# Performance work log

Measured on AMD Instinct MI355X. Metric: run time of the kernel, lower is better.

Reference implementation:

```python
import jax, jax.numpy as jnp
import numpy as np

B, S, HID = 8, 2048, 1024
H, DH = 16, 64
EPS = 1e-12  # torch F.normalize eps


def _heads(x):
    # [B,S,HID] -> [B,H,S,DH]
    return x.reshape(B, S, H, DH).transpose(0, 2, 1, 3)


def _l2norm(x):
    n = jnp.sqrt(jnp.sum(x * x, axis=-1, keepdims=True))
    return x / jnp.maximum(n, EPS)


def setup_inputs() -> dict:
    key = jax.random.key(0)
    ks = jax.random.split(key, 4)
    sc = 0.02
    return {
        "hidden_states": jax.random.normal(ks[0], (B, S, HID), jnp.float32),
        "attention_mask": jnp.zeros((B, 1, 1, S), jnp.int32),
        "Wq": jax.random.normal(ks[1], (HID, HID), jnp.float32) * sc,
        "bq": jnp.zeros((HID,), jnp.float32),
        "Wk": jax.random.normal(ks[2], (HID, HID), jnp.float32) * sc,
        "bk": jnp.zeros((HID,), jnp.float32),
        "Wv": jax.random.normal(ks[3], (HID, HID), jnp.float32) * sc,
        "bv": jnp.zeros((HID,), jnp.float32),
    }


def reference(hidden_states, attention_mask, Wq, bq, Wk, bk, Wv, bv):
    # QKV projections (nn.Linear: x @ W^T + b; here W stored as [in,out]-equivalent square)
    q = _heads(hidden_states @ Wq + bq)  # [B,H,S,DH]
    k = _heads(hidden_states @ Wk + bk)
    v = _heads(hidden_states @ Wv + bv)

    # mask == 0 -> valid token; transpose(-1,-2): [B,1,1,S] -> [B,1,S,1]
    mask = (attention_mask == 0).astype(q.dtype)            # [B,1,1,S]
    mask_t = jnp.swapaxes(mask, -1, -2)                      # [B,1,S,1]
    q = q * mask_t
    k = k * mask_t
    v = v * mask_t

    q = _l2norm(q)
    k = _l2norm(k)
    v = v / mask.sum(-1)[..., None]                          # divide by valid-token count

    if q.shape[-1] > q.shape[-2]:
        # DH > S: explicit O(S^2) path
        ctx = jnp.einsum("bhsq,bhqd->bhsd", jnp.einsum("bhse,bhqe->bhsq", q, k), v)
    else:
        # linear-attention order: Q @ (K^T V), O(S*DH^2)
        kv = jnp.einsum("bhse,bhsd->bhed", k, v)             # [B,H,DH,DH]
        ctx = jnp.einsum("bhse,bhed->bhsd", q, kv)

    return ctx.transpose(0, 2, 1, 3).reshape(B, S, HID)
```

## Files before the change

kernel.cpp:

```cpp
#include <hip/hip_runtime.h>
#include <stdint.h>

#define B_    8
#define S_    2048
#define HID_  1024
#define H_    16
#define DH_   64
#define M_    (B_ * S_)

using bf16x8 = __attribute__((ext_vector_type(8))) __bf16;
using bf16x4 = __attribute__((ext_vector_type(4))) __bf16;
using f32x4  = __attribute__((ext_vector_type(4))) float;

__device__ __forceinline__ void gload_lds16(const void* g, void* l) {
  __builtin_amdgcn_global_load_lds(
      (const __attribute__((address_space(1))) void*)g,
      (__attribute__((address_space(3))) void*)l, 16, 0, 0);
}

__global__ void cast_hs(const float* __restrict__ hs, __bf16* __restrict__ out, int n8) {
  int i = blockIdx.x * blockDim.x + threadIdx.x;
  int stride = gridDim.x * blockDim.x;
  for (; i < n8; i += stride) {
    const float4* p = (const float4*)(hs + (size_t)i * 8);
    float4 a = p[0], c = p[1];
    bf16x8 v;
    v[0] = (__bf16)a.x; v[1] = (__bf16)a.y; v[2] = (__bf16)a.z; v[3] = (__bf16)a.w;
    v[4] = (__bf16)c.x; v[5] = (__bf16)c.y; v[6] = (__bf16)c.z; v[7] = (__bf16)c.w;
    *(bf16x8*)(out + (size_t)i * 8) = v;
  }
}

__global__ void transpose_w(const float* __restrict__ Wq, const float* __restrict__ Wk,
                            const float* __restrict__ Wv, __bf16* __restrict__ Wt) {
  __shared__ float tile[32][33];
  int w = blockIdx.z;
  const float* W = (w == 0) ? Wq : (w == 1) ? Wk : Wv;
  int k0 = blockIdx.x * 32, n0 = blockIdx.y * 32;
  int tx = threadIdx.x, ty = threadIdx.y;
#pragma unroll
  for (int i = 0; i < 4; ++i)
    tile[ty * 4 + i][tx] = W[(size_t)(k0 + ty * 4 + i) * HID_ + n0 + tx];
  __syncthreads();
#pragma unroll
  for (int i = 0; i < 4; ++i)
    Wt[(size_t)w * HID_ * HID_ + (size_t)(n0 + ty * 4 + i) * HID_ + k0 + tx] =
        (__bf16)tile[tx][ty * 4 + i];
}

__global__ void mask_prep(const int* __restrict__ mask, float* __restrict__ validf,
                          float* __restrict__ counts) {
  __shared__ float red[256];
  int b = blockIdx.x;
  float cnt = 0.f;
  for (int s = threadIdx.x; s < S_; s += 256) {
    float v = (mask[b * S_ + s] == 0) ? 1.f : 0.f;
    validf[b * S_ + s] = v;
    cnt += v;
  }
  red[threadIdx.x] = cnt;
  __syncthreads();
  for (int off = 128; off > 0; off >>= 1) {
    if (threadIdx.x < off) red[threadIdx.x] += red[threadIdx.x + off];
    __syncthreads();
  }
  if (threadIdx.x == 0) counts[b] = red[0];
}

__global__ __launch_bounds__(512, 2) void qkv_gemm8(
    const __bf16* __restrict__ hsb, const __bf16* __restrict__ Wt,
    const float* __restrict__ biasq, const float* __restrict__ biask,
    const float* __restrict__ biasv, const float* __restrict__ validf,
    const float* __restrict__ counts, __bf16* __restrict__ qn,
    __bf16* __restrict__ kT, __bf16* __restrict__ vT) {
  __shared__ __bf16 As[2][2][128 * 64];
  __shared__ __bf16 Bs[2][2][128 * 64];

  int bid = blockIdx.x;
  int swz = (bid & 7) * 96 + (bid >> 3);
  int tm = swz / 12;
  int tnw = swz - tm * 12;
  int tn = tnw & 3;
  int w  = tnw >> 2;

  int tid = threadIdx.x;
  int lane = tid & 63, wid = tid >> 6;
  int lr = lane & 15, g = lane >> 4;
  int wr = wid >> 2, wcn = wid & 3;

  int m0 = tm * 256, n0 = tn * 256;
  const __bf16* Bsrc = Wt + (size_t)w * (HID_ * HID_);

  int srow = tid >> 3;
  int scol = ((tid & 7) ^ (srow & 7)) << 3;
  int soff = tid * 16;

  auto stA = [&](int t_, int ah) {
    const __bf16* s0 = hsb + (size_t)(m0 + ah * 128 + srow) * HID_ + t_ * 64 + scol;
    char* d = (char*)&As[t_ & 1][ah][0] + soff;
    gload_lds16(s0, d);
    gload_lds16(s0 + (size_t)64 * HID_, d + 8192);
  };
  auto stB = [&](int t_, int bh) {
    const __bf16* s0 = Bsrc + (size_t)(n0 + bh * 128 + srow) * HID_ + t_ * 64 + scol;
    char* d = (char*)&Bs[t_ & 1][bh][0] + soff;
    gload_lds16(s0, d);
    gload_lds16(s0 + (size_t)64 * HID_, d + 8192);
  };

  int swz8 = (lr & 7) << 4;
  int arow = wr * 64 + lr;
  int brow = (wcn & 1) * 64 + lr;
  int bsel = wcn >> 1;

  f32x4 acc[8][4] = {};
  bf16x8 fb[4], fbN[4], fa0[4], fa1[4];

#define RD_A(DST, BUF, MH, KK)                                                \
  _Pragma("unroll")                                                           \
  for (int mf = 0; mf < 4; ++mf)                                              \
    DST[mf] = *(const bf16x8*)((const char*)&As[BUF][MH][0] +                 \
                               (arow + mf * 16) * 128 +                       \
                               (((KK) * 64 + g * 16) ^ swz8));                \
  __builtin_amdgcn_sched_barrier(0);

#define RD_B(DST, BUF, KK)                                                    \
  _Pragma("unroll")                                                           \
  for (int nf = 0; nf < 4; ++nf)                                              \
    DST[nf] = *(const bf16x8*)((const char*)&Bs[BUF][bsel][0] +               \
                               (brow + nf * 16) * 128 +                       \
                               (((KK) * 64 + g * 16) ^ swz8));                \
  __builtin_amdgcn_sched_barrier(0);

#define CLUSTER(ACCB, FA, FB, LG)                                             \
  asm volatile("s_waitcnt lgkmcnt(" #LG ")" ::: "memory");                    \
  __builtin_amdgcn_sched_barrier(0);                                          \
  __builtin_amdgcn_s_setprio(1);                                              \
  _Pragma("unroll")                                                           \
  for (int mf = 0; mf < 4; ++mf)                                              \
    _Pragma("unroll")                                                         \
    for (int nf = 0; nf < 4; ++nf)                                            \
      acc[(ACCB) + mf][nf] = __builtin_amdgcn_mfma_f32_16x16x32_bf16(         \
          FA[mf], FB[nf], acc[(ACCB) + mf][nf], 0, 0, 0);                     \
  __builtin_amdgcn_s_setprio(0);                                              \
  __builtin_amdgcn_sched_barrier(0);

  stA(0, 0); stA(0, 1); stB(0, 0); stB(0, 1);

#pragma unroll 2
  for (int t = 0; t < 16; ++t) {
    int buf = t & 1;
    asm volatile("s_waitcnt vmcnt(0)" ::: "memory");
    __builtin_amdgcn_s_barrier();
    __builtin_amdgcn_sched_barrier(0);

    RD_B(fb,  buf, 0);
    RD_A(fa0, buf, 0, 0);
    RD_A(fa1, buf, 1, 0);
    if (t < 15) { stA(t + 1, 0); stA(t + 1, 1); }

    CLUSTER(0, fa0, fb, 4)

    RD_B(fbN, buf, 1);
    RD_A(fa0, buf, 0, 1);
    if (t < 15) stB(t + 1, 0);

    CLUSTER(4, fa1, fb, 8)

    RD_A(fa1, buf, 1, 1);
    if (t < 15) stB(t + 1, 1);

    CLUSTER(0, fa0, fbN, 4)
    CLUSTER(4, fa1, fbN, 0)
  }
#undef RD_A
#undef RD_B
#undef CLUSTER

  const float* bias = (w == 0) ? biasq : (w == 1) ? biask : biasv;
  float bb[4];
#pragma unroll
  for (int nf = 0; nf < 4; ++nf) bb[nf] = bias[n0 + wcn * 64 + nf * 16 + lr];

  int batch = m0 >> 11;
  float invcnt = 1.0f / counts[batch];
  int h = tn * 4 + wcn;

#pragma unroll
  for (int m = 0; m < 8; ++m) {
    int mh = m >> 2, mf = m & 3;
    int rbase = m0 + mh * 128 + wr * 64 + mf * 16 + g * 4;
    float vld[4];
#pragma unroll
    for (int j = 0; j < 4; ++j) vld[j] = validf[rbase + j];
    float ss[4] = {0.f, 0.f, 0.f, 0.f};
#pragma unroll
    for (int nf = 0; nf < 4; ++nf)
#pragma unroll
      for (int j = 0; j < 4; ++j) {
        float x = (acc[m][nf][j] + bb[nf]) * vld[j];
        acc[m][nf][j] = x;
        ss[j] += x * x;
      }
    float sc[4];
#pragma unroll
    for (int j = 0; j < 4; ++j) {
      float s = ss[j];
      s += __shfl_xor(s, 1);
      s += __shfl_xor(s, 2);
      s += __shfl_xor(s, 4);
      s += __shfl_xor(s, 8);
      if (w == 2) sc[j] = vld[j] * invcnt;
      else        sc[j] = 1.0f / fmaxf(sqrtf(s), 1e-12f);
    }
    if (w == 0) {
#pragma unroll
      for (int nf = 0; nf < 4; ++nf) {
        int c = n0 + wcn * 64 + nf * 16 + lr;
#pragma unroll
        for (int j = 0; j < 4; ++j)
          qn[(size_t)(rbase + j) * HID_ + c] = (__bf16)(acc[m][nf][j] * sc[j]);
      }
    } else {
      __bf16* dst = (w == 1) ? kT : vT;
      int sbase = rbase & (S_ - 1);
#pragma unroll
      for (int nf = 0; nf < 4; ++nf) {
        int d = nf * 16 + lr;
        bf16x4 pk;
#pragma unroll
        for (int j = 0; j < 4; ++j) pk[j] = (__bf16)(acc[m][nf][j] * sc[j]);
        *(bf16x4*)(dst + (size_t)((batch * H_ + h) * DH_ + d) * S_ + sbase) = pk;
      }
    }
  }
}

__global__ __launch_bounds__(256) void kv_gemm(const __bf16* __restrict__ kT,
                                               const __bf16* __restrict__ vT,
                                               __bf16* __restrict__ vk) {
  __shared__ __align__(16) char smem[65536];
  __bf16* kbuf = (__bf16*)smem;
  __bf16* vbuf = (__bf16*)(smem + 32768);

  int bh = blockIdx.x;
  int tid = threadIdx.x, lane = tid & 63, wid = tid >> 6;
  int g = lane >> 4, lr = lane & 15;
  const __bf16* kb = kT + (size_t)bh * DH_ * S_;
  const __bf16* vb = vT + (size_t)bh * DH_ * S_;

  f32x4 acc[4][4] = {};

  for (int sc0 = 0; sc0 < S_; sc0 += 256) {
#pragma unroll
    for (int it = 0; it < 8; ++it) {
      int seg = tid + it * 256;
      int row = seg >> 5, col = (seg & 31) * 8;
      gload_lds16(kb + (size_t)row * S_ + sc0 + col, (void*)(kbuf + seg * 8));
      gload_lds16(vb + (size_t)row * S_ + sc0 + col, (void*)(vbuf + seg * 8));
    }
    __syncthreads();
    int sl = wid * 64;
#pragma unroll
    for (int kk = 0; kk < 64; kk += 32) {
      bf16x8 fa[4], fb[4];
#pragma unroll
      for (int m = 0; m < 4; ++m)
        fa[m] = *(const bf16x8*)(vbuf + (m * 16 + lr) * 256 + sl + kk + g * 8);
#pragma unroll
      for (int n = 0; n < 4; ++n)
        fb[n] = *(const bf16x8*)(kbuf + (n * 16 + lr) * 256 + sl + kk + g * 8);
#pragma unroll
      for (int m = 0; m < 4; ++m)
#pragma unroll
        for (int n = 0; n < 4; ++n)
          acc[m][n] = __builtin_amdgcn_mfma_f32_16x16x32_bf16(fa[m], fb[n], acc[m][n], 0, 0, 0);
    }
    __syncthreads();
  }

  float* red = (float*)smem;
#pragma unroll
  for (int m = 0; m < 4; ++m)
#pragma unroll
    for (int n = 0; n < 4; ++n)
#pragma unroll
      for (int j = 0; j < 4; ++j)
        red[wid * 4096 + (m * 16 + g * 4 + j) * 64 + n * 16 + lr] = acc[m][n][j];
  __syncthreads();
  for (int idx = tid; idx < 4096; idx += 256) {
    float s = red[idx] + red[4096 + idx] + red[8192 + idx] + red[12288 + idx];
    vk[(size_t)bh * 4096 + idx] = (__bf16)s;
  }
}

__global__ __launch_bounds__(256) void ctx_gemm(const __bf16* __restrict__ qn,
                                                const __bf16* __restrict__ vk,
                                                float* __restrict__ out) {
  __shared__ __align__(16) __bf16 qbuf[128 * 64];
  __shared__ __align__(16) __bf16 wbuf[64 * 64];

  int st = blockIdx.x;
  int bh = blockIdx.y;
  int b = bh >> 4, h = bh & 15;
  int tid = threadIdx.x, lane = tid & 63, wid = tid >> 6;
  int g = lane >> 4, lr = lane & 15;
  int s0 = st * 128;

#pragma unroll
  for (int it = 0; it < 4; ++it) {
    int seg = tid + it * 256;
    int row = seg >> 3, col = (seg & 7) * 8;
    gload_lds16(qn + (size_t)(b * S_ + s0 + row) * HID_ + h * DH_ + col,
                (void*)(qbuf + seg * 8));
  }
#pragma unroll
  for (int it = 0; it < 2; ++it) {
    int seg = tid + it * 256;
    gload_lds16(vk + (size_t)bh * 4096 + seg * 8, (void*)(wbuf + seg * 8));
  }
  __syncthreads();

  f32x4 acc[2][4] = {};
#pragma unroll
  for (int kk = 0; kk < 64; kk += 32) {
    bf16x8 fa[2], fb[4];
#pragma unroll
    for (int m = 0; m < 2; ++m)
      fa[m] = *(const bf16x8*)(qbuf + (wid * 32 + m * 16 + lr) * 64 + kk + g * 8);
#pragma unroll
    for (int n = 0; n < 4; ++n)
      fb[n] = *(const bf16x8*)(wbuf + (n * 16 + lr) * 64 + kk + g * 8);
#pragma unroll
    for (int m = 0; m < 2; ++m)
#pragma unroll
      for (int n = 0; n < 4; ++n)
        acc[m][n] = __builtin_amdgcn_mfma_f32_16x16x32_bf16(fa[m], fb[n], acc[m][n], 0, 0, 0);
  }

#pragma unroll
  for (int m = 0; m < 2; ++m) {
    int rbase = s0 + wid * 32 + m * 16 + g * 4;
#pragma unroll
    for (int n = 0; n < 4; ++n) {
      int d = n * 16 + lr;
#pragma unroll
      for (int j = 0; j < 4; ++j)
        out[(size_t)(b * S_ + rbase + j) * HID_ + h * DH_ + d] = acc[m][n][j];
    }
  }
}

extern "C" void kernel_launch(void* const* d_in, const int* in_sizes, int n_in,
                              void* d_out, int out_size, void* d_ws, size_t ws_size,
                              hipStream_t stream) {
  const float* hs   = (const float*)d_in[0];
  const int*   mask = (const int*)d_in[1];
  const float* Wq   = (const float*)d_in[2];
  const float* bq   = (const float*)d_in[3];
  const float* Wk   = (const float*)d_in[4];
  const float* bk   = (const float*)d_in[5];
  const float* Wv   = (const float*)d_in[6];
  const float* bv   = (const float*)d_in[7];
  float* out = (float*)d_out;

  char* ws = (char*)d_ws;
  __bf16* hsb    = (__bf16*)(ws);
  __bf16* Wt     = (__bf16*)(ws + (33554432));
  __bf16* qn     = (__bf16*)(ws + (41943040));
  __bf16* kT     = (__bf16*)(ws + (75497472));
  __bf16* vT     = (__bf16*)(ws + (109051904));
  __bf16* vk     = (__bf16*)(ws + (142606336));
  float*  validf = (float*)(ws + (143654912));
  float*  counts = (float*)(ws + (143654912) + 65536);

  cast_hs<<<2048, 256, 0, stream>>>(hs, hsb, (B_ * S_ * HID_) / 8);
  transpose_w<<<dim3(32, 32, 3), dim3(32, 8), 0, stream>>>(Wq, Wk, Wv, Wt);
  mask_prep<<<8, 256, 0, stream>>>(mask, validf, counts);
  qkv_gemm8<<<768, 512, 0, stream>>>(hsb, Wt, bq, bk, bv, validf, counts, qn, kT, vT);
  kv_gemm<<<128, 256, 0, stream>>>(kT, vT, vk);
  ctx_gemm<<<dim3(16, 128), 256, 0, stream>>>(qn, vk, out);
}
```

Before: 184.9 us.

## Load GEMM B operand directly to registers and split kv_gemm over sequence halves

```diff
diff --git a/kernel.cpp b/kernel.cpp
--- a/kernel.cpp
+++ b/kernel.cpp
@@ -74,7 +74,6 @@
     const float* __restrict__ counts, __bf16* __restrict__ qn,
     __bf16* __restrict__ kT, __bf16* __restrict__ vT) {
   __shared__ __bf16 As[2][2][128 * 64];
-  __shared__ __bf16 Bs[2][2][128 * 64];
 
   int bid = blockIdx.x;
   int swz = (bid & 7) * 96 + (bid >> 3);
@@ -101,20 +100,17 @@
     gload_lds16(s0, d);
     gload_lds16(s0 + (size_t)64 * HID_, d + 8192);
   };
-  auto stB = [&](int t_, int bh) {
-    const __bf16* s0 = Bsrc + (size_t)(n0 + bh * 128 + srow) * HID_ + t_ * 64 + scol;
-    char* d = (char*)&Bs[t_ & 1][bh][0] + soff;
-    gload_lds16(s0, d);
-    gload_lds16(s0 + (size_t)64 * HID_, d + 8192);
-  };
 
   int swz8 = (lr & 7) << 4;
   int arow = wr * 64 + lr;
-  int brow = (wcn & 1) * 64 + lr;
-  int bsel = wcn >> 1;
+
+  const __bf16* bp[4];
+#pragma unroll
+  for (int nf = 0; nf < 4; ++nf)
+    bp[nf] = Bsrc + (size_t)(n0 + wcn * 64 + nf * 16 + lr) * HID_ + g * 8;
 
   f32x4 acc[8][4] = {};
-  bf16x8 fb[4], fbN[4], fa0[4], fa1[4];
+  bf16x8 fa[4], fab[4], fbX[4], fbY[4], fbN[4];
 
 #define RD_A(DST, BUF, MH, KK)                                                \
   _Pragma("unroll")                                                           \
@@ -124,15 +120,7 @@
                                (((KK) * 64 + g * 16) ^ swz8));                \
   __builtin_amdgcn_sched_barrier(0);
 
-#define RD_B(DST, BUF, KK)                                                    \
-  _Pragma("unroll")                                                           \
-  for (int nf = 0; nf < 4; ++nf)                                              \
-    DST[nf] = *(const bf16x8*)((const char*)&Bs[BUF][bsel][0] +               \
-                               (brow + nf * 16) * 128 +                       \
-                               (((KK) * 64 + g * 16) ^ swz8));                \
-  __builtin_amdgcn_sched_barrier(0);
-
-#define CLUSTER(ACCB, FA, FB, LG)                                             \
+#define CLUSTER(ACCB, FA, FB, LG)                                            \
   asm volatile("s_waitcnt lgkmcnt(" #LG ")" ::: "memory");                    \
   __builtin_amdgcn_sched_barrier(0);                                          \
   __builtin_amdgcn_s_setprio(1);                                              \
@@ -145,37 +133,44 @@
   __builtin_amdgcn_s_setprio(0);                                              \
   __builtin_amdgcn_sched_barrier(0);
 
-  stA(0, 0); stA(0, 1); stB(0, 0); stB(0, 1);
-
-#pragma unroll 2
-  for (int t = 0; t < 16; ++t) {
-    int buf = t & 1;
-    asm volatile("s_waitcnt vmcnt(0)" ::: "memory");
-    __builtin_amdgcn_s_barrier();
-    __builtin_amdgcn_sched_barrier(0);
-
-    RD_B(fb,  buf, 0);
-    RD_A(fa0, buf, 0, 0);
-    RD_A(fa1, buf, 1, 0);
-    if (t < 15) { stA(t + 1, 0); stA(t + 1, 1); }
-
-    CLUSTER(0, fa0, fb, 4)
-
-    RD_B(fbN, buf, 1);
-    RD_A(fa0, buf, 0, 1);
-    if (t < 15) stB(t + 1, 0);
-
-    CLUSTER(4, fa1, fb, 8)
-
-    RD_A(fa1, buf, 1, 1);
-    if (t < 15) stB(t + 1, 1);
-
-    CLUSTER(0, fa0, fbN, 4)
-    CLUSTER(4, fa1, fbN, 0)
+#define STEP(T, BUF, FBC, FBP)                                                \
+  {                                                                           \
+    asm volatile("s_waitcnt vmcnt(0)" ::: "memory");                          \
+    __builtin_amdgcn_s_barrier();                                             \
+    __builtin_amdgcn_sched_barrier(0);                                        \
+    _Pragma("unroll")                                                         \
+    for (int nf = 0; nf < 4; ++nf)                                            \
+      fbN[nf] = *(const bf16x8*)(bp[nf] + (T) * 64 + 32);                     \
+    __builtin_amdgcn_sched_barrier(0);                                        \
+    RD_A(fa,  BUF, 0, 0)                                                      \
+    RD_A(fab, BUF, 0, 1)                                                      \
+    if ((T) < 15) stA((T) + 1, 0);                                            \
+    CLUSTER(0, fa, FBC, 4)                                                    \
+    CLUSTER(0, fab, fbN, 0)                                                   \
+    RD_A(fa,  BUF, 1, 0)                                                      \
+    RD_A(fab, BUF, 1, 1)                                                      \
+    if ((T) < 15) {                                                           \
+      stA((T) + 1, 1);                                                        \
+      _Pragma("unroll")                                                       \
+      for (int nf = 0; nf < 4; ++nf)                                          \
+        FBP[nf] = *(const bf16x8*)(bp[nf] + ((T) + 1) * 64);                  \
+    }                                                                         \
+    __builtin_amdgcn_sched_barrier(0);                                        \
+    CLUSTER(4, fa, FBC, 4)                                                    \
+    CLUSTER(4, fab, fbN, 0)                                                   \
+  }
+
+  stA(0, 0); stA(0, 1);
+#pragma unroll
+  for (int nf = 0; nf < 4; ++nf) fbX[nf] = *(const bf16x8*)(bp[nf]);
+
+  for (int t2 = 0; t2 < 16; t2 += 2) {
+    STEP(t2,     0, fbX, fbY)
+    STEP(t2 + 1, 1, fbY, fbX)
   }
 #undef RD_A
-#undef RD_B
 #undef CLUSTER
+#undef STEP
 
   const float* bias = (w == 0) ? biasq : (w == 1) ? biask : biasv;
   float bb[4];
@@ -238,12 +233,12 @@
 
 __global__ __launch_bounds__(256) void kv_gemm(const __bf16* __restrict__ kT,
                                                const __bf16* __restrict__ vT,
-                                               __bf16* __restrict__ vk) {
+                                               float* __restrict__ vkp) {
   __shared__ __align__(16) char smem[65536];
   __bf16* kbuf = (__bf16*)smem;
   __bf16* vbuf = (__bf16*)(smem + 32768);
 
-  int bh = blockIdx.x;
+  int bh = blockIdx.x & 127, half = blockIdx.x >> 7;
   int tid = threadIdx.x, lane = tid & 63, wid = tid >> 6;
   int g = lane >> 4, lr = lane & 15;
   const __bf16* kb = kT + (size_t)bh * DH_ * S_;
@@ -251,7 +246,8 @@
 
   f32x4 acc[4][4] = {};
 
-  for (int sc0 = 0; sc0 < S_; sc0 += 256) {
+  int sbeg = half * (S_ / 2);
+  for (int sc0 = sbeg; sc0 < sbeg + S_ / 2; sc0 += 256) {
 #pragma unroll
     for (int it = 0; it < 8; ++it) {
       int seg = tid + it * 256;
@@ -290,8 +286,14 @@
   __syncthreads();
   for (int idx = tid; idx < 4096; idx += 256) {
     float s = red[idx] + red[4096 + idx] + red[8192 + idx] + red[12288 + idx];
-    vk[(size_t)bh * 4096 + idx] = (__bf16)s;
-  }
+    vkp[(size_t)(half * 128 + bh) * 4096 + idx] = s;
+  }
+}
+
+__global__ __launch_bounds__(256) void vk_reduce(const float* __restrict__ vkp,
+                                                 __bf16* __restrict__ vk) {
+  int i = blockIdx.x * 256 + threadIdx.x;
+  vk[i] = (__bf16)(vkp[i] + vkp[524288 + i]);
 }
 
 __global__ __launch_bounds__(256) void ctx_gemm(const __bf16* __restrict__ qn,
@@ -373,11 +375,13 @@
   __bf16* vk     = (__bf16*)(ws + (142606336));
   float*  validf = (float*)(ws + (143654912));
   float*  counts = (float*)(ws + (143654912) + 65536);
+  float*  vkp    = (float*)(ws + (33554432));
 
   cast_hs<<<2048, 256, 0, stream>>>(hs, hsb, (B_ * S_ * HID_) / 8);
   transpose_w<<<dim3(32, 32, 3), dim3(32, 8), 0, stream>>>(Wq, Wk, Wv, Wt);
   mask_prep<<<8, 256, 0, stream>>>(mask, validf, counts);
   qkv_gemm8<<<768, 512, 0, stream>>>(hsb, Wt, bq, bk, bv, validf, counts, qn, kT, vT);
-  kv_gemm<<<128, 256, 0, stream>>>(kT, vT, vk);
+  kv_gemm<<<256, 256, 0, stream>>>(kT, vT, vkp);
+  vk_reduce<<<2048, 256, 0, stream>>>(vkp, vk);
   ctx_gemm<<<dim3(16, 128), 256, 0, stream>>>(qn, vk, out);
 }
```

New measurement: 223.8 us, median of 4. 21.0% more time.

## Merge prep kernels into one launch and split kv_gemm over sequence halves

Applied to the files above, without the earlier changes.

```diff
diff --git a/kernel.cpp b/kernel.cpp
--- a/kernel.cpp
+++ b/kernel.cpp
@@ -18,53 +18,58 @@
       (__attribute__((address_space(3))) void*)l, 16, 0, 0);
 }
 
-__global__ void cast_hs(const float* __restrict__ hs, __bf16* __restrict__ out, int n8) {
-  int i = blockIdx.x * blockDim.x + threadIdx.x;
-  int stride = gridDim.x * blockDim.x;
-  for (; i < n8; i += stride) {
-    const float4* p = (const float4*)(hs + (size_t)i * 8);
-    float4 a = p[0], c = p[1];
-    bf16x8 v;
-    v[0] = (__bf16)a.x; v[1] = (__bf16)a.y; v[2] = (__bf16)a.z; v[3] = (__bf16)a.w;
-    v[4] = (__bf16)c.x; v[5] = (__bf16)c.y; v[6] = (__bf16)c.z; v[7] = (__bf16)c.w;
-    *(bf16x8*)(out + (size_t)i * 8) = v;
-  }
-}
-
-__global__ void transpose_w(const float* __restrict__ Wq, const float* __restrict__ Wk,
-                            const float* __restrict__ Wv, __bf16* __restrict__ Wt) {
-  __shared__ float tile[32][33];
-  int w = blockIdx.z;
-  const float* W = (w == 0) ? Wq : (w == 1) ? Wk : Wv;
-  int k0 = blockIdx.x * 32, n0 = blockIdx.y * 32;
-  int tx = threadIdx.x, ty = threadIdx.y;
-#pragma unroll
-  for (int i = 0; i < 4; ++i)
-    tile[ty * 4 + i][tx] = W[(size_t)(k0 + ty * 4 + i) * HID_ + n0 + tx];
-  __syncthreads();
-#pragma unroll
-  for (int i = 0; i < 4; ++i)
-    Wt[(size_t)w * HID_ * HID_ + (size_t)(n0 + ty * 4 + i) * HID_ + k0 + tx] =
-        (__bf16)tile[tx][ty * 4 + i];
-}
-
-__global__ void mask_prep(const int* __restrict__ mask, float* __restrict__ validf,
-                          float* __restrict__ counts) {
-  __shared__ float red[256];
-  int b = blockIdx.x;
-  float cnt = 0.f;
-  for (int s = threadIdx.x; s < S_; s += 256) {
-    float v = (mask[b * S_ + s] == 0) ? 1.f : 0.f;
-    validf[b * S_ + s] = v;
-    cnt += v;
-  }
-  red[threadIdx.x] = cnt;
-  __syncthreads();
-  for (int off = 128; off > 0; off >>= 1) {
-    if (threadIdx.x < off) red[threadIdx.x] += red[threadIdx.x + off];
+__global__ __launch_bounds__(256) void prep(
+    const float* __restrict__ hs, __bf16* __restrict__ hsb,
+    const float* __restrict__ Wq, const float* __restrict__ Wk,
+    const float* __restrict__ Wv, __bf16* __restrict__ Wt,
+    const int* __restrict__ mask, float* __restrict__ validf,
+    float* __restrict__ counts) {
+  int bid = blockIdx.x;
+  int tid = threadIdx.x;
+  if (bid < 2048) {
+    int n8 = (B_ * S_ * HID_) / 8;
+    int i = bid * 256 + tid;
+    int stride = 2048 * 256;
+    for (; i < n8; i += stride) {
+      const float4* p = (const float4*)(hs + (size_t)i * 8);
+      float4 a = p[0], c = p[1];
+      bf16x8 v;
+      v[0] = (__bf16)a.x; v[1] = (__bf16)a.y; v[2] = (__bf16)a.z; v[3] = (__bf16)a.w;
+      v[4] = (__bf16)c.x; v[5] = (__bf16)c.y; v[6] = (__bf16)c.z; v[7] = (__bf16)c.w;
+      *(bf16x8*)(hsb + (size_t)i * 8) = v;
+    }
+  } else if (bid < 5120) {
+    __shared__ float tile[32][33];
+    int idx = bid - 2048;
+    int w = idx >> 10, r = idx & 1023;
+    int k0 = (r & 31) * 32, n0 = (r >> 5) * 32;
+    const float* W = (w == 0) ? Wq : (w == 1) ? Wk : Wv;
+    int tx = tid & 31, ty = tid >> 5;
+#pragma unroll
+    for (int i = 0; i < 4; ++i)
+      tile[ty * 4 + i][tx] = W[(size_t)(k0 + ty * 4 + i) * HID_ + n0 + tx];
     __syncthreads();
-  }
-  if (threadIdx.x == 0) counts[b] = red[0];
+#pragma unroll
+    for (int i = 0; i < 4; ++i)
+      Wt[(size_t)w * HID_ * HID_ + (size_t)(n0 + ty * 4 + i) * HID_ + k0 + tx] =
+          (__bf16)tile[tx][ty * 4 + i];
+  } else {
+    __shared__ float red[256];
+    int b = bid - 5120;
+    float cnt = 0.f;
+    for (int s = tid; s < S_; s += 256) {
+      float v = (mask[b * S_ + s] == 0) ? 1.f : 0.f;
+      validf[b * S_ + s] = v;
+      cnt += v;
+    }
+    red[tid] = cnt;
+    __syncthreads();
+    for (int off = 128; off > 0; off >>= 1) {
+      if (tid < off) red[tid] += red[tid + off];
+      __syncthreads();
+    }
+    if (tid == 0) counts[b] = red[0];
+  }
 }
 
 __global__ __launch_bounds__(512, 2) void qkv_gemm8(
@@ -238,12 +243,12 @@
 
 __global__ __launch_bounds__(256) void kv_gemm(const __bf16* __restrict__ kT,
                                                const __bf16* __restrict__ vT,
-                                               __bf16* __restrict__ vk) {
+                                               float* __restrict__ vkp) {
   __shared__ __align__(16) char smem[65536];
   __bf16* kbuf = (__bf16*)smem;
   __bf16* vbuf = (__bf16*)(smem + 32768);
 
-  int bh = blockIdx.x;
+  int bh = blockIdx.x & 127, half = blockIdx.x >> 7;
   int tid = threadIdx.x, lane = tid & 63, wid = tid >> 6;
   int g = lane >> 4, lr = lane & 15;
   const __bf16* kb = kT + (size_t)bh * DH_ * S_;
@@ -251,7 +256,8 @@
 
   f32x4 acc[4][4] = {};
 
-  for (int sc0 = 0; sc0 < S_; sc0 += 256) {
+  int sbeg = half * (S_ / 2);
+  for (int sc0 = sbeg; sc0 < sbeg + S_ / 2; sc0 += 256) {
 #pragma unroll
     for (int it = 0; it < 8; ++it) {
       int seg = tid + it * 256;
@@ -290,12 +296,12 @@
   __syncthreads();
   for (int idx = tid; idx < 4096; idx += 256) {
     float s = red[idx] + red[4096 + idx] + red[8192 + idx] + red[12288 + idx];
-    vk[(size_t)bh * 4096 + idx] = (__bf16)s;
+    vkp[(size_t)(half * 128 + bh) * 4096 + idx] = s;
   }
 }
 
 __global__ __launch_bounds__(256) void ctx_gemm(const __bf16* __restrict__ qn,
-                                                const __bf16* __restrict__ vk,
+                                                const float* __restrict__ vkp,
                                                 float* __restrict__ out) {
   __shared__ __align__(16) __bf16 qbuf[128 * 64];
   __shared__ __align__(16) __bf16 wbuf[64 * 64];
@@ -314,10 +320,24 @@
     gload_lds16(qn + (size_t)(b * S_ + s0 + row) * HID_ + h * DH_ + col,
                 (void*)(qbuf + seg * 8));
   }
-#pragma unroll
-  for (int it = 0; it < 2; ++it) {
-    int seg = tid + it * 256;
-    gload_lds16(vk + (size_t)bh * 4096 + seg * 8, (void*)(wbuf + seg * 8));
+  {
+    const float* p0 = vkp + (size_t)bh * 4096;
+    const float* p1 = p0 + 524288;
+#pragma unroll
+    for (int it = 0; it < 2; ++it) {
+      int i = tid * 8 + it * 2048;
+      f32x4 a0 = *(const f32x4*)(p0 + i);
+      f32x4 a1 = *(const f32x4*)(p0 + i + 4);
+      f32x4 c0 = *(const f32x4*)(p1 + i);
+      f32x4 c1 = *(const f32x4*)(p1 + i + 4);
+      bf16x8 v;
+#pragma unroll
+      for (int j = 0; j < 4; ++j) {
+        v[j]     = (__bf16)(a0[j] + c0[j]);
+        v[4 + j] = (__bf16)(a1[j] + c1[j]);
+      }
+      *(bf16x8*)(wbuf + i) = v;
+    }
   }
   __syncthreads();
 
@@ -370,14 +390,12 @@
   __bf16* qn     = (__bf16*)(ws + (41943040));
   __bf16* kT     = (__bf16*)(ws + (75497472));
   __bf16* vT     = (__bf16*)(ws + (109051904));
-  __bf16* vk     = (__bf16*)(ws + (142606336));
   float*  validf = (float*)(ws + (143654912));
   float*  counts = (float*)(ws + (143654912) + 65536);
-
-  cast_hs<<<2048, 256, 0, stream>>>(hs, hsb, (B_ * S_ * HID_) / 8);
-  transpose_w<<<dim3(32, 32, 3), dim3(32, 8), 0, stream>>>(Wq, Wk, Wv, Wt);
-  mask_prep<<<8, 256, 0, stream>>>(mask, validf, counts);
+  float*  vkp    = (float*)(ws + (33554432));
+
+  prep<<<5128, 256, 0, stream>>>(hs, hsb, Wq, Wk, Wv, Wt, mask, validf, counts);
   qkv_gemm8<<<768, 512, 0, stream>>>(hsb, Wt, bq, bk, bv, validf, counts, qn, kT, vT);
-  kv_gemm<<<128, 256, 0, stream>>>(kT, vT, vk);
-  ctx_gemm<<<dim3(16, 128), 256, 0, stream>>>(qn, vk, out);
-}
+  kv_gemm<<<256, 256, 0, stream>>>(kT, vT, vkp);
+  ctx_gemm<<<dim3(16, 128), 256, 0, stream>>>(qn, vkp, out);
+}
```

Result: faster. 176.8 us, median of 3 (-4.4%).
